# Kernel tuning notes

Measured on AMD Instinct MI355X. Metric: run time of the kernel, lower is better.

## Reference

```python
import jax, jax.numpy as jnp
import numpy as np

B, N = 512, 100000

def skew(t):
    # t: (B,3) -> (B,3,3) cross-product matrix [t]_x
    z = jnp.zeros_like(t[:, 0])
    return jnp.stack([
        jnp.stack([z, -t[:, 2], t[:, 1]], axis=-1),
        jnp.stack([t[:, 2], z, -t[:, 0]], axis=-1),
        jnp.stack([-t[:, 1], t[:, 0], z], axis=-1),
    ], axis=-2)

def rt_to_e(models):
    # models: (B,3,4) = [R | t]; E = [t]_x @ R
    R = models[..., :3]
    t = models[..., 3]
    return skew(t) @ R

def setup_inputs() -> dict:
    key = jax.random.key(0)
    k1, k2 = jax.random.split(key)
    models = jax.random.normal(k1, (B, 3, 4), dtype=jnp.float32)
    points = jax.random.normal(k2, (N, 4), dtype=jnp.float32)
    K1 = jnp.ones((3, 3), dtype=jnp.float32)
    K2 = jnp.ones((3, 3), dtype=jnp.float32)
    return {"models": models, "points": points, "K1": K1, "K2": K2}

def reference(models, points, K1, K2):
    # threshold=None path: derive thr from focal lengths
    f1 = (K1[0, 0] + K1[1, 1]) / 2
    f2 = (K2[0, 0] + K2[1, 1]) / 2
    thr = (1.0 / f1 + 1.0 / f2) / 2

    n = points.shape[0]
    ones = jnp.ones((n, 1), dtype=points.dtype)
    hom1 = jnp.concatenate([points[:, 0:2], ones], axis=-1)  # (N,3)
    hom2 = jnp.concatenate([points[:, 2:4], ones], axis=-1)  # (N,3)

    E = rt_to_e(models)  # (B,3,3)
    M_x1 = jnp.einsum('bij,nj->bin', E, hom1)  # E  @ x1^T : (B,3,N)
    M_x2 = jnp.einsum('bji,nj->bin', E, hom2)  # E^T @ x2^T : (B,3,N)

    JJ_T = M_x1[:, 0]**2 + M_x1[:, 1]**2 + M_x2[:, 0]**2 + M_x2[:, 1]**2  # (B,N)
    x1_M_x2 = jnp.einsum('ni,bin->bn', hom1, M_x2)  # (B,N)

    squared_distances = jnp.square(x1_M_x2) / JJ_T  # Sampson squared distance
    return 1.0 - jnp.clip(squared_distances / (thr * thr), 0.0, 1.0)
```

## Files before the change

kernel.cpp:

```cpp
#include <hip/hip_runtime.h>

typedef float floatx2 __attribute__((ext_vector_type(2)));
typedef float floatx4 __attribute__((ext_vector_type(4)));

constexpr int BLOCK = 256;
constexpr int PPT   = 4;
constexpr int MPB   = 32;

static __device__ __forceinline__ floatx2 fma2(floatx2 a, floatx2 b, floatx2 c) {
    return __builtin_elementwise_fma(a, b, c);
}

__global__ __launch_bounds__(BLOCK) void essential_msac_kernel(
    const float*  __restrict__ models,
    const float4* __restrict__ pts,
    const float*  __restrict__ K1,
    const float*  __restrict__ K2,
    float*        __restrict__ out,
    int B, int N)
{
    __shared__ float Es[MPB][9];

    const int bm0  = blockIdx.y * MPB;
    const int mEnd = min(MPB, B - bm0);

    if ((int)threadIdx.x < mEnd) {
        const float* m = models + (size_t)(bm0 + threadIdx.x) * 12;
        const float t0 = m[3], t1 = m[7], t2 = m[11];
        #pragma unroll
        for (int j = 0; j < 3; ++j) {
            const float R0 = m[0 + j], R1 = m[4 + j], R2 = m[8 + j];
            Es[threadIdx.x][0 + j] = fmaf(-t2, R1,  t1 * R2);
            Es[threadIdx.x][3 + j] = fmaf( t2, R0, -t0 * R2);
            Es[threadIdx.x][6 + j] = fmaf(-t1, R0,  t0 * R1);
        }
    }
    __syncthreads();

    const float f1 = (K1[0] + K1[4]) * 0.5f;
    const float f2 = (K2[0] + K2[4]) * 0.5f;
    const float thr  = (1.0f / f1 + 1.0f / f2) * 0.5f;
    const float thr2 = thr * thr;
    const floatx2 thr2v = { thr2,  thr2 };
    const floatx2 onev  = { 1.0f,  1.0f };
    const floatx2 nonev = { -1.0f, -1.0f };
    const floatx2 zerov = { 0.0f,  0.0f };

    const int n0 = (blockIdx.x * BLOCK + threadIdx.x) * PPT;
    if (n0 >= N) return;

    float4 p[PPT];
    #pragma unroll
    for (int k = 0; k < PPT; ++k) p[k] = pts[n0 + k];

    floatx2 px[2], py[2], pu[2], pv[2];
    #pragma unroll
    for (int g = 0; g < 2; ++g) {
        px[g] = { p[2*g].x, p[2*g+1].x };
        py[g] = { p[2*g].y, p[2*g+1].y };
        pu[g] = { p[2*g].z, p[2*g+1].z };
        pv[g] = { p[2*g].w, p[2*g+1].w };
    }

    float* o = out + (size_t)bm0 * N + n0;
    for (int mi = 0; mi < mEnd; ++mi) {
        const float* e = Es[mi];
        const floatx2 E0 = {e[0],e[0]}, E1 = {e[1],e[1]}, E2 = {e[2],e[2]};
        const floatx2 E3 = {e[3],e[3]}, E4 = {e[4],e[4]}, E5 = {e[5],e[5]};
        const floatx2 E6 = {e[6],e[6]}, E7 = {e[7],e[7]}, E8 = {e[8],e[8]};

        floatx2 rr[2];
        #pragma unroll
        for (int g = 0; g < 2; ++g) {
            const floatx2 a0 = fma2(E0, px[g], fma2(E1, py[g], E2));
            const floatx2 a1 = fma2(E3, px[g], fma2(E4, py[g], E5));
            const floatx2 b0 = fma2(E0, pu[g], fma2(E3, pv[g], E6));
            const floatx2 b1 = fma2(E1, pu[g], fma2(E4, pv[g], E7));
            const floatx2 b2 = fma2(E2, pu[g], fma2(E5, pv[g], E8));

            const floatx2 jj  = fma2(a0, a0, fma2(a1, a1, fma2(b0, b0, b1 * b1)));
            const floatx2 s   = fma2(px[g], b0, fma2(py[g], b1, b2));
            const floatx2 num = s * s;
            const floatx2 jjt = jj * thr2v;
            const floatx2 rj  = { __builtin_amdgcn_rcpf(jjt.x),
                                  __builtin_amdgcn_rcpf(jjt.y) };
            const floatx2 d   = num * rj;
            const floatx2 r   = fma2(d, nonev, onev);
            rr[g] = __builtin_elementwise_max(r, zerov);
        }

        floatx4 v4 = { rr[0].x, rr[0].y, rr[1].x, rr[1].y };
        *reinterpret_cast<floatx4*>(o) = v4;
        o += N;
    }
}

extern "C" void kernel_launch(void* const* d_in, const int* in_sizes, int n_in,
                              void* d_out, int out_size, void* d_ws, size_t ws_size,
                              hipStream_t stream)
{
    const float* models = (const float*)d_in[0];
    const float* points = (const float*)d_in[1];
    const float* K1     = (const float*)d_in[2];
    const float* K2     = (const float*)d_in[3];
    float* out = (float*)d_out;

    const int B = in_sizes[0] / 12;
    const int N = in_sizes[1] / 4;

    dim3 grid((N + BLOCK * PPT - 1) / (BLOCK * PPT), (B + MPB - 1) / MPB);
    essential_msac_kernel<<<grid, BLOCK, 0, stream>>>(
        models, (const float4*)points, K1, K2, out, B, N);
}
```

Measured before the change: 40.12 us.

## Retile so each wave owns four models in registers and sixteen points per lane

Each wavefront now computes its four essential matrices directly in registers, which removes the shared-memory table and the block barrier. Each lane processes four sub-tiles of four points, so every block covers 1024 points by 16 models instead of 1024 points by 32 models, and the grid gains more blocks along the model axis. The idea is to raise per-thread work and drop the sync, at the cost of redundant E computation per lane and higher register pressure. Tail handling switches to clamped loads and guarded scalar stores.

```diff
diff --git a/kernel.cpp b/kernel.cpp
--- a/kernel.cpp
+++ b/kernel.cpp
@@ -4,8 +4,10 @@
 typedef float floatx4 __attribute__((ext_vector_type(4)));
 
 constexpr int BLOCK = 256;
-constexpr int PPT   = 4;
-constexpr int MPB   = 32;
+constexpr int MPW   = 4;
+constexpr int SUB   = 4;
+constexpr int TILE_PTS = 64 * 4 * SUB;
+constexpr int MPB   = 4 * MPW;
 
 static __device__ __forceinline__ floatx2 fma2(floatx2 a, floatx2 b, floatx2 c) {
     return __builtin_elementwise_fma(a, b, c);
@@ -19,23 +21,24 @@
     float*        __restrict__ out,
     int B, int N)
 {
-    __shared__ float Es[MPB][9];
+    const int wq   = threadIdx.x >> 6;
+    const int lane = threadIdx.x & 63;
+    const int bm   = blockIdx.y * MPB + wq * MPW;
 
-    const int bm0  = blockIdx.y * MPB;
-    const int mEnd = min(MPB, B - bm0);
-
-    if ((int)threadIdx.x < mEnd) {
-        const float* m = models + (size_t)(bm0 + threadIdx.x) * 12;
+    const float* mm = models + (size_t)bm * 12;
+    float E[MPW][9];
+    #pragma unroll
+    for (int mi = 0; mi < MPW; ++mi) {
+        const float* m = mm + mi * 12;
         const float t0 = m[3], t1 = m[7], t2 = m[11];
         #pragma unroll
         for (int j = 0; j < 3; ++j) {
             const float R0 = m[0 + j], R1 = m[4 + j], R2 = m[8 + j];
-            Es[threadIdx.x][0 + j] = fmaf(-t2, R1,  t1 * R2);
-            Es[threadIdx.x][3 + j] = fmaf( t2, R0, -t0 * R2);
-            Es[threadIdx.x][6 + j] = fmaf(-t1, R0,  t0 * R1);
+            E[mi][0 + j] = fmaf(-t2, R1,  t1 * R2);
+            E[mi][3 + j] = fmaf( t2, R0, -t0 * R2);
+            E[mi][6 + j] = fmaf(-t1, R0,  t0 * R1);
         }
     }
-    __syncthreads();
 
     const float f1 = (K1[0] + K1[4]) * 0.5f;
     const float f2 = (K2[0] + K2[4]) * 0.5f;
@@ -46,52 +49,65 @@
     const floatx2 nonev = { -1.0f, -1.0f };
     const floatx2 zerov = { 0.0f,  0.0f };
 
-    const int n0 = (blockIdx.x * BLOCK + threadIdx.x) * PPT;
-    if (n0 >= N) return;
-
-    float4 p[PPT];
+    const int nb = blockIdx.x * TILE_PTS + lane * 4;
+    floatx2 px[SUB][2], py[SUB][2], pu[SUB][2], pv[SUB][2];
     #pragma unroll
-    for (int k = 0; k < PPT; ++k) p[k] = pts[n0 + k];
-
-    floatx2 px[2], py[2], pu[2], pv[2];
-    #pragma unroll
-    for (int g = 0; g < 2; ++g) {
-        px[g] = { p[2*g].x, p[2*g+1].x };
-        py[g] = { p[2*g].y, p[2*g+1].y };
-        pu[g] = { p[2*g].z, p[2*g+1].z };
-        pv[g] = { p[2*g].w, p[2*g+1].w };
+    for (int s = 0; s < SUB; ++s) {
+        const int n0s = nb + s * 256;
+        float4 p[4];
+        #pragma unroll
+        for (int k = 0; k < 4; ++k) {
+            const int idx = min(n0s + k, N - 1);
+            p[k] = pts[idx];
+        }
+        #pragma unroll
+        for (int g = 0; g < 2; ++g) {
+            px[s][g] = { p[2*g].x, p[2*g+1].x };
+            py[s][g] = { p[2*g].y, p[2*g+1].y };
+            pu[s][g] = { p[2*g].z, p[2*g+1].z };
+            pv[s][g] = { p[2*g].w, p[2*g+1].w };
+        }
     }
 
-    float* o = out + (size_t)bm0 * N + n0;
-    for (int mi = 0; mi < mEnd; ++mi) {
-        const float* e = Es[mi];
+    #pragma unroll
+    for (int mi = 0; mi < MPW; ++mi) {
+        const float* e = E[mi];
         const floatx2 E0 = {e[0],e[0]}, E1 = {e[1],e[1]}, E2 = {e[2],e[2]};
         const floatx2 E3 = {e[3],e[3]}, E4 = {e[4],e[4]}, E5 = {e[5],e[5]};
         const floatx2 E6 = {e[6],e[6]}, E7 = {e[7],e[7]}, E8 = {e[8],e[8]};
+        float* orow = out + (size_t)(bm + mi) * N;
 
-        floatx2 rr[2];
         #pragma unroll
-        for (int g = 0; g < 2; ++g) {
-            const floatx2 a0 = fma2(E0, px[g], fma2(E1, py[g], E2));
-            const floatx2 a1 = fma2(E3, px[g], fma2(E4, py[g], E5));
-            const floatx2 b0 = fma2(E0, pu[g], fma2(E3, pv[g], E6));
-            const floatx2 b1 = fma2(E1, pu[g], fma2(E4, pv[g], E7));
-            const floatx2 b2 = fma2(E2, pu[g], fma2(E5, pv[g], E8));
+        for (int s = 0; s < SUB; ++s) {
+            floatx2 rr[2];
+            #pragma unroll
+            for (int g = 0; g < 2; ++g) {
+                const floatx2 a0 = fma2(E0, px[s][g], fma2(E1, py[s][g], E2));
+                const floatx2 a1 = fma2(E3, px[s][g], fma2(E4, py[s][g], E5));
+                const floatx2 b0 = fma2(E0, pu[s][g], fma2(E3, pv[s][g], E6));
+                const floatx2 b1 = fma2(E1, pu[s][g], fma2(E4, pv[s][g], E7));
+                const floatx2 b2 = fma2(E2, pu[s][g], fma2(E5, pv[s][g], E8));
 
-            const floatx2 jj  = fma2(a0, a0, fma2(a1, a1, fma2(b0, b0, b1 * b1)));
-            const floatx2 s   = fma2(px[g], b0, fma2(py[g], b1, b2));
-            const floatx2 num = s * s;
-            const floatx2 jjt = jj * thr2v;
-            const floatx2 rj  = { __builtin_amdgcn_rcpf(jjt.x),
-                                  __builtin_amdgcn_rcpf(jjt.y) };
-            const floatx2 d   = num * rj;
-            const floatx2 r   = fma2(d, nonev, onev);
-            rr[g] = __builtin_elementwise_max(r, zerov);
+                const floatx2 jj  = fma2(a0, a0, fma2(a1, a1, fma2(b0, b0, b1 * b1)));
+                const floatx2 sv  = fma2(px[s][g], b0, fma2(py[s][g], b1, b2));
+                const floatx2 num = sv * sv;
+                const floatx2 jjt = jj * thr2v;
+                const floatx2 rj  = { __builtin_amdgcn_rcpf(jjt.x),
+                                      __builtin_amdgcn_rcpf(jjt.y) };
+                const floatx2 d   = num * rj;
+                const floatx2 r   = fma2(d, nonev, onev);
+                rr[g] = __builtin_elementwise_max(r, zerov);
+            }
+
+            const int n0s = nb + s * 256;
+            if (n0s + 4 <= N) {
+                floatx4 v4 = { rr[0].x, rr[0].y, rr[1].x, rr[1].y };
+                *reinterpret_cast<floatx4*>(orow + n0s) = v4;
+            } else {
+                const float rs[4] = { rr[0].x, rr[0].y, rr[1].x, rr[1].y };
+                for (int k = 0; k < 4 && n0s + k < N; ++k) orow[n0s + k] = rs[k];
+            }
         }
-
-        floatx4 v4 = { rr[0].x, rr[0].y, rr[1].x, rr[1].y };
-        *reinterpret_cast<floatx4*>(o) = v4;
-        o += N;
     }
 }
 
@@ -108,7 +124,8 @@
     const int B = in_sizes[0] / 12;
     const int N = in_sizes[1] / 4;
 
-    dim3 grid((N + BLOCK * PPT - 1) / (BLOCK * PPT), (B + MPB - 1) / MPB);
+    dim3 grid((N + TILE_PTS - 1) / TILE_PTS,
+              (B + MPB - 1) / MPB);
     essential_msac_kernel<<<grid, BLOCK, 0, stream>>>(
         models, (const float4*)points, K1, K2, out, B, N);
 }
```

Measured after the change: 42.63 us. +6.3%, slower.

## Split E construction into a pre-kernel and flatten output into a grid-stride loop

Applied to the files above, without the earlier changes.

Builds the essential matrices in a separate small kernel writing a padded table to workspace, then runs a persistent grid-stride kernel over the flattened B*N output. Each thread derives the model index with a magic-number division, reloads E from global/L2 and the points for every output vector. This drops the per-block shared-memory setup and __syncthreads, and gives a fixed 1024-block grid instead of the per-model loop over 32 models. In exchange it adds a second launch and per-iteration E/point reloads, which lose the register reuse of points across models. It also adds a scalar path for output vectors that straddle a row boundary.

```diff
diff --git a/kernel.cpp b/kernel.cpp
--- a/kernel.cpp
+++ b/kernel.cpp
@@ -4,39 +4,38 @@
 typedef float floatx4 __attribute__((ext_vector_type(4)));
 
 constexpr int BLOCK = 256;
-constexpr int PPT   = 4;
-constexpr int MPB   = 32;
+constexpr int GRID  = 1024;
 
 static __device__ __forceinline__ floatx2 fma2(floatx2 a, floatx2 b, floatx2 c) {
     return __builtin_elementwise_fma(a, b, c);
 }
 
-__global__ __launch_bounds__(BLOCK) void essential_msac_kernel(
-    const float*  __restrict__ models,
+__global__ void build_E_kernel(const float* __restrict__ models,
+                               float* __restrict__ Etab, int B)
+{
+    const int b = blockIdx.x * blockDim.x + threadIdx.x;
+    if (b >= B) return;
+    const float* m = models + (size_t)b * 12;
+    const float t0 = m[3], t1 = m[7], t2 = m[11];
+    float* e = Etab + b * 12;
+    #pragma unroll
+    for (int j = 0; j < 3; ++j) {
+        const float R0 = m[0 + j], R1 = m[4 + j], R2 = m[8 + j];
+        e[0 + j] = fmaf(-t2, R1,  t1 * R2);
+        e[3 + j] = fmaf( t2, R0, -t0 * R2);
+        e[6 + j] = fmaf(-t1, R0,  t0 * R1);
+    }
+    e[9] = e[10] = e[11] = 0.0f;
+}
+
+__global__ __launch_bounds__(BLOCK) void essential_dense_kernel(
+    const float4* __restrict__ Etab,
     const float4* __restrict__ pts,
     const float*  __restrict__ K1,
     const float*  __restrict__ K2,
     float*        __restrict__ out,
-    int B, int N)
+    int N, unsigned total, unsigned long long nmagic)
 {
-    __shared__ float Es[MPB][9];
-
-    const int bm0  = blockIdx.y * MPB;
-    const int mEnd = min(MPB, B - bm0);
-
-    if ((int)threadIdx.x < mEnd) {
-        const float* m = models + (size_t)(bm0 + threadIdx.x) * 12;
-        const float t0 = m[3], t1 = m[7], t2 = m[11];
-        #pragma unroll
-        for (int j = 0; j < 3; ++j) {
-            const float R0 = m[0 + j], R1 = m[4 + j], R2 = m[8 + j];
-            Es[threadIdx.x][0 + j] = fmaf(-t2, R1,  t1 * R2);
-            Es[threadIdx.x][3 + j] = fmaf( t2, R0, -t0 * R2);
-            Es[threadIdx.x][6 + j] = fmaf(-t1, R0,  t0 * R1);
-        }
-    }
-    __syncthreads();
-
     const float f1 = (K1[0] + K1[4]) * 0.5f;
     const float f2 = (K2[0] + K2[4]) * 0.5f;
     const float thr  = (1.0f / f1 + 1.0f / f2) * 0.5f;
@@ -46,52 +45,75 @@
     const floatx2 nonev = { -1.0f, -1.0f };
     const floatx2 zerov = { 0.0f,  0.0f };
 
-    const int n0 = (blockIdx.x * BLOCK + threadIdx.x) * PPT;
-    if (n0 >= N) return;
+    const unsigned stride = (unsigned)GRID * BLOCK * 4;
+    for (unsigned i0 = (blockIdx.x * BLOCK + threadIdx.x) * 4; i0 < total; i0 += stride) {
+        const unsigned b  = (unsigned)(((unsigned long long)i0 * nmagic) >> 48);
+        const unsigned n0 = i0 - b * (unsigned)N;
 
-    float4 p[PPT];
-    #pragma unroll
-    for (int k = 0; k < PPT; ++k) p[k] = pts[n0 + k];
+        floatx4 v4;
+        if (n0 <= (unsigned)(N - 4)) {
+            const float4 e0 = Etab[b * 3 + 0];
+            const float4 e1 = Etab[b * 3 + 1];
+            const float4 e2 = Etab[b * 3 + 2];
+            const floatx2 E0 = {e0.x,e0.x}, E1 = {e0.y,e0.y}, E2 = {e0.z,e0.z};
+            const floatx2 E3 = {e0.w,e0.w}, E4 = {e1.x,e1.x}, E5 = {e1.y,e1.y};
+            const floatx2 E6 = {e1.z,e1.z}, E7 = {e1.w,e1.w}, E8 = {e2.x,e2.x};
 
-    floatx2 px[2], py[2], pu[2], pv[2];
-    #pragma unroll
-    for (int g = 0; g < 2; ++g) {
-        px[g] = { p[2*g].x, p[2*g+1].x };
-        py[g] = { p[2*g].y, p[2*g+1].y };
-        pu[g] = { p[2*g].z, p[2*g+1].z };
-        pv[g] = { p[2*g].w, p[2*g+1].w };
-    }
+            float4 p[4];
+            #pragma unroll
+            for (int k = 0; k < 4; ++k) p[k] = pts[n0 + k];
 
-    float* o = out + (size_t)bm0 * N + n0;
-    for (int mi = 0; mi < mEnd; ++mi) {
-        const float* e = Es[mi];
-        const floatx2 E0 = {e[0],e[0]}, E1 = {e[1],e[1]}, E2 = {e[2],e[2]};
-        const floatx2 E3 = {e[3],e[3]}, E4 = {e[4],e[4]}, E5 = {e[5],e[5]};
-        const floatx2 E6 = {e[6],e[6]}, E7 = {e[7],e[7]}, E8 = {e[8],e[8]};
+            floatx2 rr[2];
+            #pragma unroll
+            for (int g = 0; g < 2; ++g) {
+                const floatx2 px = { p[2*g].x, p[2*g+1].x };
+                const floatx2 py = { p[2*g].y, p[2*g+1].y };
+                const floatx2 pu = { p[2*g].z, p[2*g+1].z };
+                const floatx2 pv = { p[2*g].w, p[2*g+1].w };
 
-        floatx2 rr[2];
-        #pragma unroll
-        for (int g = 0; g < 2; ++g) {
-            const floatx2 a0 = fma2(E0, px[g], fma2(E1, py[g], E2));
-            const floatx2 a1 = fma2(E3, px[g], fma2(E4, py[g], E5));
-            const floatx2 b0 = fma2(E0, pu[g], fma2(E3, pv[g], E6));
-            const floatx2 b1 = fma2(E1, pu[g], fma2(E4, pv[g], E7));
-            const floatx2 b2 = fma2(E2, pu[g], fma2(E5, pv[g], E8));
+                const floatx2 a0 = fma2(E0, px, fma2(E1, py, E2));
+                const floatx2 a1 = fma2(E3, px, fma2(E4, py, E5));
+                const floatx2 b0 = fma2(E0, pu, fma2(E3, pv, E6));
+                const floatx2 b1 = fma2(E1, pu, fma2(E4, pv, E7));
+                const floatx2 b2 = fma2(E2, pu, fma2(E5, pv, E8));
 
-            const floatx2 jj  = fma2(a0, a0, fma2(a1, a1, fma2(b0, b0, b1 * b1)));
-            const floatx2 s   = fma2(px[g], b0, fma2(py[g], b1, b2));
-            const floatx2 num = s * s;
-            const floatx2 jjt = jj * thr2v;
-            const floatx2 rj  = { __builtin_amdgcn_rcpf(jjt.x),
-                                  __builtin_amdgcn_rcpf(jjt.y) };
-            const floatx2 d   = num * rj;
-            const floatx2 r   = fma2(d, nonev, onev);
-            rr[g] = __builtin_elementwise_max(r, zerov);
+                const floatx2 jj  = fma2(a0, a0, fma2(a1, a1, fma2(b0, b0, b1 * b1)));
+                const floatx2 sv  = fma2(px, b0, fma2(py, b1, b2));
+                const floatx2 num = sv * sv;
+                const floatx2 jjt = jj * thr2v;
+                const floatx2 rj  = { __builtin_amdgcn_rcpf(jjt.x),
+                                      __builtin_amdgcn_rcpf(jjt.y) };
+                const floatx2 d   = num * rj;
+                const floatx2 r   = fma2(d, nonev, onev);
+                rr[g] = __builtin_elementwise_max(r, zerov);
+            }
+            v4 = floatx4{ rr[0].x, rr[0].y, rr[1].x, rr[1].y };
+        } else {
+            float rs[4];
+            #pragma unroll
+            for (int k = 0; k < 4; ++k) {
+                const unsigned i  = i0 + k;
+                const unsigned bb = (unsigned)(((unsigned long long)i * nmagic) >> 48);
+                const unsigned nn = i - bb * (unsigned)N;
+                const float4 e0 = Etab[bb * 3 + 0];
+                const float4 e1 = Etab[bb * 3 + 1];
+                const float4 e2 = Etab[bb * 3 + 2];
+                const float4 P  = pts[nn];
+                const float x = P.x, y = P.y, u = P.z, v = P.w;
+                const float a0 = fmaf(e0.x, x, fmaf(e0.y, y, e0.z));
+                const float a1 = fmaf(e0.w, x, fmaf(e1.x, y, e1.y));
+                const float b0 = fmaf(e0.x, u, fmaf(e0.w, v, e1.z));
+                const float b1 = fmaf(e0.y, u, fmaf(e1.x, v, e1.w));
+                const float b2 = fmaf(e0.z, u, fmaf(e1.y, v, e2.x));
+                const float jj = fmaf(a0, a0, fmaf(a1, a1, fmaf(b0, b0, b1 * b1)));
+                const float s  = fmaf(x, b0, fmaf(y, b1, b2));
+                const float d  = (s * s) * __builtin_amdgcn_rcpf(jj * thr2);
+                rs[k] = fmaxf(1.0f - d, 0.0f);
+            }
+            v4 = floatx4{ rs[0], rs[1], rs[2], rs[3] };
         }
 
-        floatx4 v4 = { rr[0].x, rr[0].y, rr[1].x, rr[1].y };
-        *reinterpret_cast<floatx4*>(o) = v4;
-        o += N;
+        *reinterpret_cast<floatx4*>(out + i0) = v4;
     }
 }
 
@@ -103,12 +125,15 @@
     const float* points = (const float*)d_in[1];
     const float* K1     = (const float*)d_in[2];
     const float* K2     = (const float*)d_in[3];
-    float* out = (float*)d_out;
+    float* out  = (float*)d_out;
+    float* Etab = (float*)d_ws;
 
     const int B = in_sizes[0] / 12;
     const int N = in_sizes[1] / 4;
+    const unsigned total = (unsigned)B * (unsigned)N;
+    const unsigned long long nmagic = ((1ULL << 48) + (unsigned)N - 1) / (unsigned)N;
 
-    dim3 grid((N + BLOCK * PPT - 1) / (BLOCK * PPT), (B + MPB - 1) / MPB);
-    essential_msac_kernel<<<grid, BLOCK, 0, stream>>>(
-        models, (const float4*)points, K1, K2, out, B, N);
+    build_E_kernel<<<(B + 255) / 256, 256, 0, stream>>>(models, Etab, B);
+    essential_dense_kernel<<<GRID, BLOCK, 0, stream>>>(
+        (const float4*)Etab, (const float4*)points, K1, K2, out, N, total, nmagic);
 }
```

After: 76.55 us. 1.91x slower.
